# Performance work log

Hardware: AMD Instinct MI355X
Metric: run time of the kernel (lower is better)

The kernel has to match this reference:

```python
import jax, jax.numpy as jnp
import numpy as np

DIMS = 1024
BATCH, SEQ = 4, 2048

def setup_inputs() -> dict:
    key = jax.random.key(0)
    k1, k2, k3, k4 = jax.random.split(key, 4)
    scale = 1.0 / np.sqrt(DIMS)
    return {
        "input_seq_embs": jax.random.normal(k1, (BATCH, SEQ, DIMS), dtype=jnp.float32),
        "Wq": jax.random.normal(k2, (DIMS, DIMS), dtype=jnp.float32) * scale,
        "Wk": jax.random.normal(k3, (DIMS, DIMS), dtype=jnp.float32) * scale,
        "Wv": jax.random.normal(k4, (DIMS, DIMS), dtype=jnp.float32) * scale,
    }

def reference(input_seq_embs, Wq, Wk, Wv):
    # nn.Linear(x) = x @ W.T ; weights stored [out, in]
    q = jnp.einsum('bsd,ed->bse', input_seq_embs, Wq)
    k = jnp.einsum('bsd,ed->bse', input_seq_embs, Wk)
    v = jnp.einsum('bsd,ed->bse', input_seq_embs, Wv)
    # full N x N scores, NO 1/sqrt(d) scaling (faithful to source)
    scores = jnp.einsum('bqe,bke->bqk', q, k)
    causal = jnp.tril(jnp.ones((q.shape[1], q.shape[1]), dtype=bool))
    scores = jnp.where(causal[None, :, :], scores, -jnp.inf)
    attn = jax.nn.softmax(scores, axis=-1)
    return jnp.einsum('bqk,bke->bqe', attn, v)
```

## Files before the change

kernel.cpp:

```cpp
#include <hip/hip_runtime.h>


typedef _Float16 h8 __attribute__((ext_vector_type(8)));
typedef _Float16 h4 __attribute__((ext_vector_type(4)));
typedef float f32x4 __attribute__((ext_vector_type(4)));

#define BM 128
#define BN 128

__device__ __forceinline__ void gl_lds16(const _Float16* g, _Float16* l) {
    __builtin_amdgcn_global_load_lds(
        (const __attribute__((address_space(1))) void*)g,
        (__attribute__((address_space(3))) void*)l, 16, 0, 0);
}


#define BARX do { asm volatile("" ::: "memory"); __builtin_amdgcn_s_barrier(); \
                  asm volatile("" ::: "memory"); } while (0)
#define VMW(n) asm volatile("s_waitcnt vmcnt(" #n ")" ::: "memory")

#define LDA4(reg, h) do { _Pragma("unroll") \
    for (int i = 0; i < 4; i++) \
        af[i] = *(const h8*)&sm[(reg) + (wmr + (h) * 64 + i * 16 + la) * 32 + sg]; } while (0)

#define LDB4(reg) do { _Pragma("unroll") \
    for (int j = 0; j < 4; j++) \
        bf[j] = *(const h8*)&sm[(reg) + (wnr + j * 16 + la) * 32 + sg]; } while (0)

#define MMP(h) do { __builtin_amdgcn_s_setprio(1); _Pragma("unroll") \
    for (int i = 0; i < 4; i++) { _Pragma("unroll") \
        for (int j = 0; j < 4; j++) \
            acc[(h) * 4 + i][j] = __builtin_amdgcn_mfma_f32_16x16x32_f16( \
                af[i], bf[j], acc[(h) * 4 + i][j], 0, 0, 0); } \
    __builtin_amdgcn_s_setprio(0); } while (0)

#define STG(gp, off, ldsoff) do { \
    gl_lds16((gp) + rA1 + (off), lbase + (ldsoff)); \
    gl_lds16((gp) + rA2 + (off), lbase + (ldsoff) + 4096); } while (0)

__global__ __launch_bounds__(512, 2) void qkv256(
    const _Float16* __restrict__ A, const _Float16* __restrict__ B,
    _Float16* __restrict__ C)
{
    __shared__ __align__(16) _Float16 sm[65536];

    const int bid = blockIdx.x;
    const int wg = (bid & 7) * 48 + (bid >> 3);
    const int by = wg / 12, bx = wg % 12;
    const int m0 = by * 256, n0 = bx * 256;

    const int tid = threadIdx.x;
    const int l = tid & 63;
    const int wv = tid >> 6;

    const int lr = l >> 2;
    const int gsrc = (l & 3) ^ ((l >> 3) & 3);
    const _Float16* gA = A + (size_t)(m0 + lr) * 1024 + gsrc * 8;
    const _Float16* gB = B + (size_t)(n0 + lr) * 1024 + gsrc * 8;
    const size_t rA1 = (size_t)(wv * 16) * 1024;
    const size_t rA2 = (size_t)((wv + 8) * 16) * 1024;
    _Float16* lbase = sm + wv * 512;

    const int la = l & 15, qd = l >> 4;
    const int sg = (qd ^ ((la >> 1) & 3)) * 8;
    const int wmr = (wv >> 2) * 128;
    const int wnr = (wv & 3) * 64;

    f32x4 acc[8][4];
    #pragma unroll
    for (int i = 0; i < 8; i++)
        #pragma unroll
        for (int j = 0; j < 4; j++)
            acc[i][j] = (f32x4){0.f, 0.f, 0.f, 0.f};

    STG(gA, 0,  0);
    STG(gB, 0,  16384);
    STG(gA, 32, 8192);
    STG(gB, 32, 24576);
    STG(gA, 64, 32768);
    STG(gB, 64, 49152);
    VMW(8);
    BARX;

    #pragma unroll 1
    for (int it = 0; it < 7; ++it) {
        h8 af[4], bf[4];
        LDB4(16384); LDA4(0, 0);      STG(gA, 96, 40960);  BARX; MMP(0); BARX;
        LDA4(0, 1);                   STG(gB, 96, 57344);  BARX; MMP(1); VMW(8); BARX;
        LDB4(24576); LDA4(8192, 0);   STG(gA, 128, 0);     BARX; MMP(0); BARX;
        LDA4(8192, 1);                STG(gB, 128, 16384); BARX; MMP(1); VMW(8); BARX;
        LDB4(49152); LDA4(32768, 0);  STG(gA, 160, 8192);  BARX; MMP(0); BARX;
        LDA4(32768, 1);               STG(gB, 160, 24576); BARX; MMP(1); VMW(8); BARX;
        LDB4(57344); LDA4(40960, 0);  STG(gA, 192, 32768); BARX; MMP(0); BARX;
        LDA4(40960, 1);               STG(gB, 192, 49152); BARX; MMP(1); VMW(8); BARX;
        gA += 128; gB += 128;
    }
    {
        h8 af[4], bf[4];
        LDB4(16384); LDA4(0, 0);      STG(gA, 96, 40960);  BARX; MMP(0); BARX;
        LDA4(0, 1);                   STG(gB, 96, 57344);  BARX; MMP(1); VMW(8); BARX;
        LDB4(24576); LDA4(8192, 0);                        BARX; MMP(0); BARX;
        LDA4(8192, 1);                                     BARX; MMP(1); VMW(4); BARX;
        LDB4(49152); LDA4(32768, 0);                       BARX; MMP(0); BARX;
        LDA4(32768, 1);                                    BARX; MMP(1); VMW(0); BARX;
        LDB4(57344); LDA4(40960, 0);                       BARX; MMP(0); BARX;
        LDA4(40960, 1);                                    BARX; MMP(1); BARX;
    }

    if (bx < 8) {
        #pragma unroll
        for (int i = 0; i < 8; i++) {
            const int m = m0 + wmr + i * 16 + qd * 4;
            #pragma unroll
            for (int j = 0; j < 4; j++) {
                const int col = n0 + wnr + j * 16 + la;
                const size_t base = (size_t)(col >> 10) * 8388608 + (col & 1023);
                #pragma unroll
                for (int rr = 0; rr < 4; rr++)
                    C[base + (size_t)(m + rr) * 1024] = (_Float16)acc[i][j][rr];
            }
        }
    } else {
        _Float16* Vt = C + (size_t)2 * 8388608;
        #pragma unroll
        for (int i = 0; i < 8; i++) {
            const int m = m0 + wmr + i * 16 + qd * 4;
            const int b = m >> 11;
            const int sl = m & 2047;
            _Float16* Vb = Vt + (size_t)b * 2097152 + sl;
            #pragma unroll
            for (int j = 0; j < 4; j++) {
                const int e = n0 - 2048 + wnr + j * 16 + la;
                h4 vv = { (_Float16)acc[i][j][0], (_Float16)acc[i][j][1],
                          (_Float16)acc[i][j][2], (_Float16)acc[i][j][3] };
                *(h4*)(Vb + (size_t)e * 2048) = vv;
            }
        }
    }
}

template<int SWZ, int OM, bool KLIM>
__global__ __launch_bounds__(256) void gemm_nt(
    const _Float16* __restrict__ A, const _Float16* __restrict__ B,
    void* __restrict__ Cp, int N, int K,
    size_t sAz, size_t sBz, size_t sCz)
{
    __shared__ __align__(16) char smem[32768];
    _Float16* As = (_Float16*)smem;
    _Float16* Bs = (_Float16*)(smem + 16384);

    int bx, by;
    if (SWZ == 1) {
        const int r = blockIdx.x & 7, q2 = blockIdx.x >> 3;
        bx = q2 >> 3;
        by = ((q2 & 7) << 3) | r;
    } else if (SWZ == 2) {
        const int r = blockIdx.x & 7, g = blockIdx.x >> 3;
        if (g <= r) { by = r;      bx = g; }
        else        { by = 15 - r; bx = g - (r + 1); }
    } else {
        const int r = blockIdx.x & 7, g = blockIdx.x >> 3;
        by = (g & 1) ? (15 - r) : r;
        bx = g >> 1;
    }

    const int tid  = threadIdx.x;
    const int lane = tid & 63;
    const int wv   = tid >> 6;
    const int m0 = by * BM, n0 = bx * BN;
    const size_t z = blockIdx.z;

    const int lr = lane >> 2;
    const int lc = ((lane & 3) ^ ((lane >> 3) & 3)) * 8;
    const _Float16* pA0 = A + z * sAz + (size_t)(m0 + wv * 16 + lr) * K + lc;
    const _Float16* pA1 = pA0 + (size_t)64 * K;
    const _Float16* pB0 = B + z * sBz + (size_t)(n0 + wv * 16 + lr) * K + lc;
    const _Float16* pB1 = pB0 + (size_t)64 * K;
    _Float16* lA0 = As + wv * 512;
    _Float16* lA1 = As + (wv + 4) * 512;
    _Float16* lB0 = Bs + wv * 512;
    _Float16* lB1 = Bs + (wv + 4) * 512;

    const int la = lane & 15;
    const int qd = lane >> 4;
    const int wm = (wv >> 1) * 64;
    const int wn = (wv & 1) * 64;
    const int sg = (qd ^ ((la >> 1) & 3)) * 8;

    f32x4 acc[4][4];
    #pragma unroll
    for (int i = 0; i < 4; i++)
        #pragma unroll
        for (int j = 0; j < 4; j++)
            acc[i][j] = (f32x4){0.f, 0.f, 0.f, 0.f};

    const int kEnd = KLIM ? (m0 + BM) : K;

    for (int k0 = 0; k0 < kEnd; k0 += 64) {
        gl_lds16(pA0,      lA0);
        gl_lds16(pA1,      lA1);
        gl_lds16(pB0,      lB0);
        gl_lds16(pB1,      lB1);
        gl_lds16(pA0 + 32, lA0 + 4096);
        gl_lds16(pA1 + 32, lA1 + 4096);
        gl_lds16(pB0 + 32, lB0 + 4096);
        gl_lds16(pB1 + 32, lB1 + 4096);
        pA0 += 64; pA1 += 64; pB0 += 64; pB1 += 64;
        __syncthreads();

        #pragma unroll
        for (int s = 0; s < 2; s++) {
            h8 af[4], bf[4];
            #pragma unroll
            for (int i = 0; i < 4; i++)
                af[i] = *(const h8*)&As[s * 4096 + (wm + i * 16 + la) * 32 + sg];
            #pragma unroll
            for (int i = 0; i < 4; i++)
                bf[i] = *(const h8*)&Bs[s * 4096 + (wn + i * 16 + la) * 32 + sg];
            #pragma unroll
            for (int i = 0; i < 4; i++)
                #pragma unroll
                for (int j = 0; j < 4; j++)
                    acc[i][j] = __builtin_amdgcn_mfma_f32_16x16x32_f16(af[i], bf[j], acc[i][j], 0, 0, 0);
        }
        __syncthreads();
    }

    if (OM == 2) {
        _Float16* C = (_Float16*)Cp;
        if (n0 < 2048) {
            #pragma unroll
            for (int i = 0; i < 4; i++)
                #pragma unroll
                for (int j = 0; j < 4; j++) {
                    const int col  = n0 + wn + j * 16 + la;
                    const size_t base = (size_t)(col >> 10) * 8388608 + (col & 1023);
                    #pragma unroll
                    for (int rr = 0; rr < 4; rr++)
                        C[base + (size_t)(m0 + wm + i * 16 + qd * 4 + rr) * 1024] =
                            (_Float16)acc[i][j][rr];
                }
        } else {
            _Float16* Vt = C + (size_t)2 * 8388608;
            #pragma unroll
            for (int i = 0; i < 4; i++) {
                const int m  = m0 + wm + i * 16 + qd * 4;
                const int b  = m >> 11;
                const int sl = m & 2047;
                _Float16* Vb = Vt + (size_t)b * 2097152 + sl;
                #pragma unroll
                for (int j = 0; j < 4; j++) {
                    const int e = n0 - 2048 + wn + j * 16 + la;
                    h4 vv = { (_Float16)acc[i][j][0], (_Float16)acc[i][j][1],
                              (_Float16)acc[i][j][2], (_Float16)acc[i][j][3] };
                    *(h4*)(Vb + (size_t)e * 2048) = vv;
                }
            }
        }
    } else {
        float* C = (float*)Cp + z * sCz;
        #pragma unroll
        for (int i = 0; i < 4; i++)
            #pragma unroll
            for (int j = 0; j < 4; j++)
                #pragma unroll
                for (int rr = 0; rr < 4; rr++)
                    C[(size_t)(m0 + wm + i * 16 + qd * 4 + rr) * N + (n0 + wn + j * 16 + la)] =
                        acc[i][j][rr];
    }
}

__global__ __launch_bounds__(256) void cvt_all(
    const float* __restrict__ x, const float* __restrict__ Wq,
    const float* __restrict__ Wk, const float* __restrict__ Wv,
    _Float16* __restrict__ x_h, _Float16* __restrict__ Wh)
{
    const int bid = blockIdx.x;
    const float* src; _Float16* dst; size_t off;
    if (bid < 4096) {
        src = x; dst = x_h; off = (size_t)bid * 2048;
    } else {
        const int b2 = bid - 4096;
        const int w = b2 >> 9;
        src = (w == 0) ? Wq : ((w == 1) ? Wk : Wv);
        dst = Wh + (size_t)w * 1048576;
        off = (size_t)(b2 & 511) * 2048;
    }
    const size_t i = off + (size_t)threadIdx.x * 8;
    float4 a = *(const float4*)(src + i);
    float4 b = *(const float4*)(src + i + 4);
    h8 o = { (_Float16)a.x, (_Float16)a.y, (_Float16)a.z, (_Float16)a.w,
             (_Float16)b.x, (_Float16)b.y, (_Float16)b.z, (_Float16)b.w };
    *(h8*)(dst + i) = o;
}

__global__ __launch_bounds__(256) void softmax_causal(const float* __restrict__ S,
                                                      _Float16* __restrict__ P)
{
    const int idx = blockIdx.x;
    const int q = idx & 2047;
    const float* Srow = S + (size_t)idx * 2048;
    _Float16* Prow = P + (size_t)idx * 2048;
    const int t = threadIdx.x;
    const int k0 = t * 8;
    const int lane = t & 63, wv = t >> 6;
    __shared__ float red[4];

    float v[8];
    const bool any = (k0 <= q);
    if (any) {
        float4 a = *(const float4*)(Srow + k0);
        float4 b = *(const float4*)(Srow + k0 + 4);
        v[0] = a.x; v[1] = a.y; v[2] = a.z; v[3] = a.w;
        v[4] = b.x; v[5] = b.y; v[6] = b.z; v[7] = b.w;
    }
    float mx = -3.4e38f;
    #pragma unroll
    for (int j = 0; j < 8; j++)
        if (any && k0 + j <= q) mx = fmaxf(mx, v[j]);
    #pragma unroll
    for (int o = 32; o > 0; o >>= 1) mx = fmaxf(mx, __shfl_down(mx, o, 64));
    if (lane == 0) red[wv] = mx;
    __syncthreads();
    const float mall = fmaxf(fmaxf(red[0], red[1]), fmaxf(red[2], red[3]));
    __syncthreads();

    float sum = 0.f;
    #pragma unroll
    for (int j = 0; j < 8; j++) {
        float e = (any && k0 + j <= q) ? __expf(v[j] - mall) : 0.f;
        v[j] = e;
        sum += e;
    }
    #pragma unroll
    for (int o = 32; o > 0; o >>= 1) sum += __shfl_down(sum, o, 64);
    if (lane == 0) red[wv] = sum;
    __syncthreads();
    const float inv = 1.f / (red[0] + red[1] + red[2] + red[3]);

    const int kceil = ((q >> 7) + 1) << 7;
    if (k0 < kceil) {
        h8 o = { (_Float16)(v[0] * inv), (_Float16)(v[1] * inv),
                 (_Float16)(v[2] * inv), (_Float16)(v[3] * inv),
                 (_Float16)(v[4] * inv), (_Float16)(v[5] * inv),
                 (_Float16)(v[6] * inv), (_Float16)(v[7] * inv) };
        *(h8*)(Prow + k0) = o;
    }
}

extern "C" void kernel_launch(void* const* d_in, const int* in_sizes, int n_in,
                              void* d_out, int out_size, void* d_ws, size_t ws_size,
                              hipStream_t stream) {
    const float* x  = (const float*)d_in[0];
    const float* Wq = (const float*)d_in[1];
    const float* Wk = (const float*)d_in[2];
    const float* Wv = (const float*)d_in[3];
    float* out = (float*)d_out;

    const size_t MiB = 1024 * 1024;
    char* ws = (char*)d_ws;
    _Float16* QKVh = (_Float16*)ws;
    _Float16* Vt   = QKVh + (size_t)2 * 8388608;
    float*    S    = (float*)(ws + 48 * MiB);
    _Float16* x_h  = (_Float16*)(ws + 48 * MiB);
    _Float16* Wh   = (_Float16*)(ws + 64 * MiB);
    _Float16* P    = (_Float16*)ws;

    const dim3 blk(256);

    cvt_all<<<dim3(5632), blk, 0, stream>>>(x, Wq, Wk, Wv, x_h, Wh);

    qkv256<<<dim3(384), dim3(512), 0, stream>>>(x_h, Wh, QKVh);

    gemm_nt<2, 0, false><<<dim3(136, 1, 4), blk, 0, stream>>>(
        QKVh, QKVh + 8388608, S, 2048, 1024,
        (size_t)2097152, (size_t)2097152, (size_t)4194304);

    softmax_causal<<<dim3(4 * 2048), blk, 0, stream>>>(S, P);

    gemm_nt<3, 0, true><<<dim3(128, 1, 4), blk, 0, stream>>>(
        P, Vt, out, 1024, 2048,
        (size_t)4194304, (size_t)2097152, (size_t)2097152);
}
```

Measured before the change: 243.5 us.

## Restructure QKV GEMM into double-buffered 64-wide K windows with new swizzle

Rewrites the QKV projection kernel's main loop. It now stages 64-wide K slices into two A/B LDS buffers, double-buffered and ping-ponged, instead of the four 32-wide slices used before. It adds an 8-way XOR swizzle for the new 64-element row stride and replaces the compiler memory clobbers with sched_barrier around barriers and waitcnts. The aim is fewer barrier phases per K element and better LDS bank behaviour, at the cost of a shallower prefetch depth and more delicate hand-ordered synchronization.

```diff
diff --git a/kernel.cpp b/kernel.cpp
--- a/kernel.cpp
+++ b/kernel.cpp
@@ -14,31 +14,52 @@
         (__attribute__((address_space(3))) void*)l, 16, 0, 0);
 }
 
-
-#define BARX do { asm volatile("" ::: "memory"); __builtin_amdgcn_s_barrier(); \
-                  asm volatile("" ::: "memory"); } while (0)
-#define VMW(n) asm volatile("s_waitcnt vmcnt(" #n ")" ::: "memory")
-
-#define LDA4(reg, h) do { _Pragma("unroll") \
+#define SBAR __builtin_amdgcn_sched_barrier(0)
+#define BARX do { SBAR; __builtin_amdgcn_s_barrier(); SBAR; } while (0)
+#define VMW(n) do { SBAR; asm volatile("s_waitcnt vmcnt(" #n ")"); SBAR; } while (0)
+
+
+#define STB(gp, BB, h) do { \
+    gl_lds16((gp) + (h) * 131072,        sm + (BB) + (h) * 8192 + wv * 1024); \
+    gl_lds16((gp) + (h) * 131072 + 8192, sm + (BB) + (h) * 8192 + wv * 1024 + 512); } while (0)
+
+#define STA(gp, AB, q) do { \
+    gl_lds16((gp) + (q) * 65536,        sm + (AB) + aldb + (q) * 4096); \
+    gl_lds16((gp) + (q) * 65536 + 8192, sm + (AB) + aldb + (q) * 4096 + 512); } while (0)
+
+#define LDA4(AB, h, ap) do { _Pragma("unroll") \
     for (int i = 0; i < 4; i++) \
-        af[i] = *(const h8*)&sm[(reg) + (wmr + (h) * 64 + i * 16 + la) * 32 + sg]; } while (0)
-
-#define LDB4(reg) do { _Pragma("unroll") \
+        af[i] = *(const h8*)&sm[(AB) + abase + (h) * 4096 + i * 1024 + (ap)]; } while (0)
+
+#define LDB4(BB, ap) do { _Pragma("unroll") \
     for (int j = 0; j < 4; j++) \
-        bf[j] = *(const h8*)&sm[(reg) + (wnr + j * 16 + la) * 32 + sg]; } while (0)
-
-#define MMP(h) do { __builtin_amdgcn_s_setprio(1); _Pragma("unroll") \
+        bf[j] = *(const h8*)&sm[(BB) + bbase + j * 1024 + (ap)]; } while (0)
+
+#define MMQ(h) do { __builtin_amdgcn_s_setprio(1); _Pragma("unroll") \
     for (int i = 0; i < 4; i++) { _Pragma("unroll") \
         for (int j = 0; j < 4; j++) \
             acc[(h) * 4 + i][j] = __builtin_amdgcn_mfma_f32_16x16x32_f16( \
                 af[i], bf[j], acc[(h) * 4 + i][j], 0, 0, 0); } \
     __builtin_amdgcn_s_setprio(0); } while (0)
 
-#define STG(gp, off, ldsoff) do { \
-    gl_lds16((gp) + rA1 + (off), lbase + (ldsoff)); \
-    gl_lds16((gp) + rA2 + (off), lbase + (ldsoff) + 4096); } while (0)
-
-__global__ __launch_bounds__(512, 2) void qkv256(
+#define WIN(AB, BB, AQ, BQ, sAp, sBp, LAST) do { h8 af[4], bf[4]; \
+    LDB4(BB, ap0); LDA4(AB, 0, ap0); \
+    if (!(LAST)) { STB(sBp, BQ, 0); VMW(2); } else { VMW(0); } \
+    BARX; MMQ(0); BARX; \
+    LDA4(AB, 1, ap0); \
+    if (!(LAST)) STB(sBp, BQ, 1); \
+    BARX; MMQ(1); BARX; \
+    LDB4(BB, ap1); LDA4(AB, 0, ap1); \
+    if (!(LAST)) STA(sAp, AQ, 0); \
+    BARX; MMQ(0); BARX; \
+    LDA4(AB, 1, ap1); \
+    if (!(LAST)) STA(sAp, AQ, 1); \
+    BARX; MMQ(1); \
+    if (!(LAST)) VMW(2); \
+    BARX; \
+} while (0)
+
+__global__ __launch_bounds__(512, 2) void qkv256c(
     const _Float16* __restrict__ A, const _Float16* __restrict__ B,
     _Float16* __restrict__ C)
 {
@@ -53,18 +74,19 @@
     const int l = tid & 63;
     const int wv = tid >> 6;
 
-    const int lr = l >> 2;
-    const int gsrc = (l & 3) ^ ((l >> 3) & 3);
-    const _Float16* gA = A + (size_t)(m0 + lr) * 1024 + gsrc * 8;
-    const _Float16* gB = B + (size_t)(n0 + lr) * 1024 + gsrc * 8;
-    const size_t rA1 = (size_t)(wv * 16) * 1024;
-    const size_t rA2 = (size_t)((wv + 8) * 16) * 1024;
-    _Float16* lbase = sm + wv * 512;
+    const int pseg = ((l & 7) ^ ((l >> 3) & 7)) * 8;
+    const _Float16* gA =
+        A + (size_t)(m0 + (wv >> 2) * 128 + (wv & 3) * 16 + (l >> 3)) * 1024 + pseg;
+    const _Float16* gB = B + (size_t)(n0 + wv * 16 + (l >> 3)) * 1024 + pseg;
+    const int aldb = (wv >> 2) * 8192 + (wv & 3) * 1024;
 
     const int la = l & 15, qd = l >> 4;
-    const int sg = (qd ^ ((la >> 1) & 3)) * 8;
-    const int wmr = (wv >> 2) * 128;
-    const int wnr = (wv & 3) * 64;
+    const int wm = (wv >> 2) * 128;
+    const int wn = (wv & 3) * 64;
+    const int ap0 = ((qd) ^ (la & 7)) * 8;
+    const int ap1 = ((4 + qd) ^ (la & 7)) * 8;
+    const int abase = (wm + la) * 64;
+    const int bbase = (wn + la) * 64;
 
     f32x4 acc[8][4];
     #pragma unroll
@@ -73,47 +95,30 @@
         for (int j = 0; j < 4; j++)
             acc[i][j] = (f32x4){0.f, 0.f, 0.f, 0.f};
 
-    STG(gA, 0,  0);
-    STG(gB, 0,  16384);
-    STG(gA, 32, 8192);
-    STG(gB, 32, 24576);
-    STG(gA, 64, 32768);
-    STG(gB, 64, 49152);
-    VMW(8);
+    STB(gB, 32768, 0); STB(gB, 32768, 1);
+    STA(gA, 0, 0);     STA(gA, 0, 1);
+    VMW(2);
     BARX;
 
+    const _Float16* sA = gA + 64;
+    const _Float16* sB = gB + 64;
+
     #pragma unroll 1
-    for (int it = 0; it < 7; ++it) {
-        h8 af[4], bf[4];
-        LDB4(16384); LDA4(0, 0);      STG(gA, 96, 40960);  BARX; MMP(0); BARX;
-        LDA4(0, 1);                   STG(gB, 96, 57344);  BARX; MMP(1); VMW(8); BARX;
-        LDB4(24576); LDA4(8192, 0);   STG(gA, 128, 0);     BARX; MMP(0); BARX;
-        LDA4(8192, 1);                STG(gB, 128, 16384); BARX; MMP(1); VMW(8); BARX;
-        LDB4(49152); LDA4(32768, 0);  STG(gA, 160, 8192);  BARX; MMP(0); BARX;
-        LDA4(32768, 1);               STG(gB, 160, 24576); BARX; MMP(1); VMW(8); BARX;
-        LDB4(57344); LDA4(40960, 0);  STG(gA, 192, 32768); BARX; MMP(0); BARX;
-        LDA4(40960, 1);               STG(gB, 192, 49152); BARX; MMP(1); VMW(8); BARX;
-        gA += 128; gB += 128;
-    }
-    {
-        h8 af[4], bf[4];
-        LDB4(16384); LDA4(0, 0);      STG(gA, 96, 40960);  BARX; MMP(0); BARX;
-        LDA4(0, 1);                   STG(gB, 96, 57344);  BARX; MMP(1); VMW(8); BARX;
-        LDB4(24576); LDA4(8192, 0);                        BARX; MMP(0); BARX;
-        LDA4(8192, 1);                                     BARX; MMP(1); VMW(4); BARX;
-        LDB4(49152); LDA4(32768, 0);                       BARX; MMP(0); BARX;
-        LDA4(32768, 1);                                    BARX; MMP(1); VMW(0); BARX;
-        LDB4(57344); LDA4(40960, 0);                       BARX; MMP(0); BARX;
-        LDA4(40960, 1);                                    BARX; MMP(1); BARX;
-    }
+    for (int t = 0; t < 14; t += 2) {
+        WIN(0, 32768, 16384, 49152, sA, sB, 0);
+        WIN(16384, 49152, 0, 32768, sA + 64, sB + 64, 0);
+        sA += 128; sB += 128;
+    }
+    WIN(0, 32768, 16384, 49152, sA, sB, 0);
+    WIN(16384, 49152, 0, 32768, sA, sB, 1);
 
     if (bx < 8) {
         #pragma unroll
         for (int i = 0; i < 8; i++) {
-            const int m = m0 + wmr + i * 16 + qd * 4;
+            const int m = m0 + wm + i * 16 + qd * 4;
             #pragma unroll
             for (int j = 0; j < 4; j++) {
-                const int col = n0 + wnr + j * 16 + la;
+                const int col = n0 + wn + j * 16 + la;
                 const size_t base = (size_t)(col >> 10) * 8388608 + (col & 1023);
                 #pragma unroll
                 for (int rr = 0; rr < 4; rr++)
@@ -124,13 +129,13 @@
         _Float16* Vt = C + (size_t)2 * 8388608;
         #pragma unroll
         for (int i = 0; i < 8; i++) {
-            const int m = m0 + wmr + i * 16 + qd * 4;
+            const int m = m0 + wm + i * 16 + qd * 4;
             const int b = m >> 11;
             const int sl = m & 2047;
             _Float16* Vb = Vt + (size_t)b * 2097152 + sl;
             #pragma unroll
             for (int j = 0; j < 4; j++) {
-                const int e = n0 - 2048 + wnr + j * 16 + la;
+                const int e = n0 - 2048 + wn + j * 16 + la;
                 h4 vv = { (_Float16)acc[i][j][0], (_Float16)acc[i][j][1],
                           (_Float16)acc[i][j][2], (_Float16)acc[i][j][3] };
                 *(h4*)(Vb + (size_t)e * 2048) = vv;
@@ -370,7 +375,7 @@
 
     cvt_all<<<dim3(5632), blk, 0, stream>>>(x, Wq, Wk, Wv, x_h, Wh);
 
-    qkv256<<<dim3(384), dim3(512), 0, stream>>>(x_h, Wh, QKVh);
+    qkv256c<<<dim3(384), dim3(512), 0, stream>>>(x_h, Wh, QKVh);
 
     gemm_nt<2, 0, false><<<dim3(136, 1, 4), blk, 0, stream>>>(
         QKVh, QKVh + 8388608, S, 2048, 1024,
```

Result: no change. 242.0 us (-0.6%).
